# Optimization experiments

Hardware: AMD Instinct MI355X
Metric: run time of the kernel (lower is better)

The kernel has to match this reference:

```python
import jax, jax.numpy as jnp
import numpy as np

B, N, L, D, H = 2, 2048, 2048, 1024, 16
HD = D // H  # 64


def setup_inputs() -> dict:
    key = jax.random.key(0)
    ks = jax.random.split(key, 12)
    s = 0.02
    return {
        "x_q": jax.random.normal(ks[0], (B, N, D), jnp.float32),
        "x_kv": jax.random.normal(ks[1], (B, L, D), jnp.float32),
        "pad_mask": jax.random.randint(ks[2], (B, L), 0, 2) > 0,
        "wq": jax.random.normal(ks[3], (D, D), jnp.float32) * s,
        "bq": jnp.zeros((D,), jnp.float32),
        "wk": jax.random.normal(ks[4], (D, D), jnp.float32) * s,
        "bk": jnp.zeros((D,), jnp.float32),
        "wv": jax.random.normal(ks[5], (D, D), jnp.float32) * s,
        "bv": jnp.zeros((D,), jnp.float32),
        "wo": jax.random.normal(ks[6], (D, D), jnp.float32) * s,
        "bo": jnp.zeros((D,), jnp.float32),
    }


def reference(x_q, x_kv, pad_mask, wq, bq, wk, bk, wv, bv, wo, bo):
    scale = HD ** -0.5
    # projections: (B, S, D) -> (B, H, S, HD)
    def split_heads(x):
        return x.reshape(x.shape[0], x.shape[1], H, HD).transpose(0, 2, 1, 3)
    q = split_heads(x_q @ wq + bq) * scale
    k = split_heads(x_kv @ wk + bk)
    v = split_heads(x_kv @ wv + bv)
    attn = jnp.einsum('bhic,bhjc->bhij', q, k)  # (B, H, N, L)
    neg = -jnp.finfo(attn.dtype).max
    attn = jnp.where(pad_mask[:, None, None, :], neg, attn)
    attn = jax.nn.softmax(attn, axis=-1)
    o = jnp.einsum('bhij,bhjc->bhic', attn, v)  # (B, H, N, HD)
    o = o.transpose(0, 2, 1, 3).reshape(B, N, D)
    return o @ wo + bo
```

## Files before the change

kernel.cpp:

```cpp
#include <hip/hip_runtime.h>
#include <hip/hip_bf16.h>
#include <math.h>

typedef __bf16 bf16;
typedef __attribute__((ext_vector_type(8))) __bf16 bf16x8;
typedef __attribute__((ext_vector_type(4))) __bf16 bf16x4;
typedef __attribute__((ext_vector_type(4))) float floatx4;
typedef __attribute__((ext_vector_type(16))) float floatx16;

#define BB 2
#define NN 2048
#define LL 2048
#define DD 1024
#define HH 16
#define HDD 64

#define QSCALE (0.125f * 1.44269504f)
#define PCLAMP 21.66f
#define MBIAS  (-100000.0f)

__device__ __forceinline__ void async16(const bf16* g, bf16* l) {
  __builtin_amdgcn_global_load_lds((const __attribute__((address_space(1))) void*)(g),
                                   (__attribute__((address_space(3))) void*)(l), 16, 0, 0);
}

__device__ __forceinline__ unsigned cvtpk(float a, float b) {
  unsigned r;
  asm("v_cvt_pk_bf16_f32 %0, %1, %2" : "=v"(r) : "v"(a), "v"(b));
  return r;
}

__device__ __forceinline__ void plswap(unsigned &x, unsigned &y) {
  auto r = __builtin_amdgcn_permlane32_swap(x, y, false, false);
  x = (unsigned)r[0];
  y = (unsigned)r[1];
}

__device__ __forceinline__ bf16x8 mk_frag(unsigned w0, unsigned w1, unsigned w2, unsigned w3) {
  union { unsigned u[4]; bf16x8 b; } f;
  f.u[0] = w0; f.u[1] = w1; f.u[2] = w2; f.u[3] = w3;
  return f.b;
}

__global__ __launch_bounds__(256) void prep_kernel(
    const float* __restrict__ xq, const float* __restrict__ xkv,
    bf16* __restrict__ Xqb, bf16* __restrict__ Xkvb, int nconv, int elemsEach,
    const float* __restrict__ W0, const float* __restrict__ W1,
    const float* __restrict__ W2, const float* __restrict__ W3,
    bf16* __restrict__ T0, bf16* __restrict__ T1,
    bf16* __restrict__ T2, bf16* __restrict__ T3,
    const unsigned* __restrict__ mask, float* __restrict__ biasF)
{
  __shared__ bf16 Tb[64][72];
  const int bid = blockIdx.x;
  const int t = threadIdx.x;

  if (bid < nconv) {
    const int half = nconv >> 1;
    const float* s = (bid < half) ? xq : xkv;
    bf16* d = (bid < half) ? Xqb : Xkvb;
    int gid = (bid < half) ? bid : bid - half;
    int idx = (gid * 256 + t) * 8;
    if (idx >= elemsEach) return;
    floatx4 a = *(const floatx4*)&s[idx];
    floatx4 b = *(const floatx4*)&s[idx + 4];
    bf16x8 o;
#pragma unroll
    for (int e = 0; e < 4; e++) { o[e] = (bf16)a[e]; o[4 + e] = (bf16)b[e]; }
    *(bf16x8*)&d[idx] = o;
    return;
  }
  if (bid < nconv + 1024) {
    const int wb = bid - nconv;
    const int which = wb >> 8;
    const float* W = which == 0 ? W0 : which == 1 ? W1 : which == 2 ? W2 : W3;
    bf16*       T = which == 0 ? T0 : which == 1 ? T1 : which == 2 ? T2 : T3;
    const int tile = wb & 255;
    const int k0 = (tile >> 4) * 64, n0 = (tile & 15) * 64;
    const int r = t >> 2;
    const int c = (t & 3) * 16;
    const float* Wr = W + (size_t)(k0 + r) * 1024 + n0 + c;
    floatx4 f0 = *(const floatx4*)(Wr + 0);
    floatx4 f1 = *(const floatx4*)(Wr + 4);
    floatx4 f2 = *(const floatx4*)(Wr + 8);
    floatx4 f3 = *(const floatx4*)(Wr + 12);
#pragma unroll
    for (int e = 0; e < 4; e++) {
      Tb[c + e][r]      = (bf16)f0[e];
      Tb[c + 4 + e][r]  = (bf16)f1[e];
      Tb[c + 8 + e][r]  = (bf16)f2[e];
      Tb[c + 12 + e][r] = (bf16)f3[e];
    }
    __syncthreads();
    bf16* Tr = T + (size_t)(n0 + r) * 1024 + k0 + c;
    *(bf16x8*)&Tr[0] = *(const bf16x8*)&Tb[r][c];
    *(bf16x8*)&Tr[8] = *(const bf16x8*)&Tb[r][c + 8];
    return;
  }
  __shared__ int hasBig, hasFloat;
  if (t == 0) { hasBig = 0; hasFloat = 0; }
  __syncthreads();
  int big = 0, flt = 0;
  for (int idx = t; idx < 1024; idx += 256) {
    unsigned v = mask[idx];
    if (v == 0x3F800000u) flt = 1;
    else if (v > 1u) big = 1;
  }
  if (big) atomicOr(&hasBig, 1);
  if (flt) atomicOr(&hasFloat, 1);
  __syncthreads();
  const int mode = hasFloat ? 2 : (hasBig ? 1 : 0);
  for (int k = t * 16; k < t * 16 + 16; k++) {
    bool m;
    if (mode == 0)      m = ((const int*)mask)[k] != 0;
    else if (mode == 1) m = ((const unsigned char*)mask)[k] != 0;
    else                m = ((const float*)mask)[k] != 0.0f;
    biasF[k] = m ? MBIAS : 0.0f;
  }
}

template <typename TC>
__device__ __forceinline__ void gemm_body32(
    int bx, const bf16* __restrict__ A, const bf16* __restrict__ Wt,
    const float* __restrict__ bias, TC* __restrict__ C, float scale, int transv)
{
  __shared__ bf16 As[128 * 64];
  __shared__ bf16 Bs[128 * 64];

  const int tm = bx >> 3, tn = bx & 7;
  const int m0 = tm * 128, n0 = tn * 128;
  const int t = threadIdx.x;
  const int w = t >> 6, l = t & 63;
  const int col = l & 31, half = l >> 5;
  const int wm = (w >> 1) * 64, wn = (w & 1) * 64;
  const int sr  = t >> 3;
  const int scl = (t & 7) * 8;
  const int scs = (((t & 7) ^ (sr & 7)) * 8);
  const int csw = col & 7;

  floatx16 acc[2][2];
#pragma unroll
  for (int mi = 0; mi < 2; mi++)
#pragma unroll
    for (int ni = 0; ni < 2; ni++)
#pragma unroll
      for (int e = 0; e < 16; e++) acc[mi][ni][e] = 0.0f;

  for (int k0 = 0; k0 < 1024; k0 += 64) {
    __syncthreads();
#pragma unroll
    for (int j = 0; j < 4; j++)
      async16(&A[(size_t)(m0 + j * 32 + sr) * 1024 + k0 + scs], &As[(j * 32 + sr) * 64 + scl]);
#pragma unroll
    for (int j = 0; j < 4; j++)
      async16(&Wt[(size_t)(n0 + j * 32 + sr) * 1024 + k0 + scs], &Bs[(j * 32 + sr) * 64 + scl]);
    __syncthreads();
#pragma unroll
    for (int kk = 0; kk < 4; kk++) {
      const int ch = ((kk * 2 + half) ^ csw) * 8;
      bf16x8 af[2], bfr[2];
#pragma unroll
      for (int mi = 0; mi < 2; mi++)
        af[mi] = *(const bf16x8*)&As[(wm + mi * 32 + col) * 64 + ch];
#pragma unroll
      for (int ni = 0; ni < 2; ni++)
        bfr[ni] = *(const bf16x8*)&Bs[(wn + ni * 32 + col) * 64 + ch];
#pragma unroll
      for (int mi = 0; mi < 2; mi++)
#pragma unroll
        for (int ni = 0; ni < 2; ni++)
          acc[mi][ni] = __builtin_amdgcn_mfma_f32_32x32x16_bf16(af[mi], bfr[ni], acc[mi][ni], 0, 0, 0);
    }
  }
#pragma unroll
  for (int ni = 0; ni < 2; ni++) {
    int colg = n0 + wn + ni * 32 + col;
    float bv = bias[colg];
#pragma unroll
    for (int mi = 0; mi < 2; mi++) {
      int rbase = m0 + wm + mi * 32 + half * 4;
      if (transv) {
#pragma unroll
        for (int g = 0; g < 4; g++) {
          int key0 = rbase + g * 8;
          int bb = key0 >> 11, key = key0 & 2047;
          bf16x4 v4;
#pragma unroll
          for (int r = 0; r < 4; r++) v4[r] = (bf16)(acc[mi][ni][g * 4 + r] + bv);
          *(bf16x4*)&((bf16*)C)[(size_t)bb * (DD * (size_t)LL) + (size_t)colg * LL + key] = v4;
        }
      } else {
#pragma unroll
        for (int g = 0; g < 4; g++)
#pragma unroll
          for (int r = 0; r < 4; r++)
            C[(size_t)(rbase + g * 8 + r) * 1024 + colg] = (TC)((acc[mi][ni][g * 4 + r] + bv) * scale);
      }
    }
  }
}

__global__ __launch_bounds__(256) void qkv_gemm32(
    const bf16* __restrict__ Xq, const bf16* __restrict__ Xkv,
    const bf16* __restrict__ Wtq, const bf16* __restrict__ Wtk, const bf16* __restrict__ Wtv,
    const float* __restrict__ bq, const float* __restrict__ bk, const float* __restrict__ bv,
    bf16* __restrict__ Qp, bf16* __restrict__ Kp, bf16* __restrict__ VtG, int shift)
{
  const int bid = blockIdx.x;
  const int which = bid >> shift;
  const int bx = bid & ((1 << shift) - 1);
  if (which == 0)      gemm_body32<bf16>(bx, Xq,  Wtq, bq, Qp,  QSCALE, 0);
  else if (which == 1) gemm_body32<bf16>(bx, Xkv, Wtk, bk, Kp,  1.0f,   0);
  else                 gemm_body32<bf16>(bx, Xkv, Wtv, bv, VtG, 1.0f,   1);
}

__global__ __launch_bounds__(256) void out_gemm(
    const bf16* __restrict__ A, const bf16* __restrict__ Wt,
    const float* __restrict__ bias, float* __restrict__ C)
{
  __shared__ bf16 As[128 * 64];
  __shared__ bf16 Bs[64 * 64];

  const int bx = blockIdx.x;
  const int tm = bx >> 4, tn = bx & 15;
  const int m0 = tm * 128, n0 = tn * 64;
  const int t = threadIdx.x;
  const int w = t >> 6, l = t & 63;
  const int q = l >> 4, i = l & 15;
  const int wm = (w >> 1) * 64, wn = (w & 1) * 32;
  const int sr  = t >> 3;
  const int scl = (t & 7) * 8;
  const int scs = (((t & 7) ^ (sr & 7)) * 8);
  const int isw = i & 7;

  const floatx4 zero = {0.f, 0.f, 0.f, 0.f};
  floatx4 acc[4][2];
#pragma unroll
  for (int mi = 0; mi < 4; mi++)
#pragma unroll
    for (int ni = 0; ni < 2; ni++) acc[mi][ni] = zero;

  for (int k0 = 0; k0 < 1024; k0 += 64) {
    __syncthreads();
#pragma unroll
    for (int j = 0; j < 4; j++)
      async16(&A[(size_t)(m0 + j * 32 + sr) * 1024 + k0 + scs], &As[(j * 32 + sr) * 64 + scl]);
#pragma unroll
    for (int j = 0; j < 2; j++)
      async16(&Wt[(size_t)(n0 + j * 32 + sr) * 1024 + k0 + scs], &Bs[(j * 32 + sr) * 64 + scl]);
    __syncthreads();
#pragma unroll
    for (int ks = 0; ks < 2; ks++) {
      const int ch = ((ks * 4 + q) ^ isw) * 8;
      bf16x8 af[4], bfr[2];
#pragma unroll
      for (int mi = 0; mi < 4; mi++)
        af[mi] = *(const bf16x8*)&As[(wm + mi * 16 + i) * 64 + ch];
#pragma unroll
      for (int ni = 0; ni < 2; ni++)
        bfr[ni] = *(const bf16x8*)&Bs[(wn + ni * 16 + i) * 64 + ch];
#pragma unroll
      for (int mi = 0; mi < 4; mi++)
#pragma unroll
        for (int ni = 0; ni < 2; ni++)
          acc[mi][ni] = __builtin_amdgcn_mfma_f32_16x16x32_bf16(af[mi], bfr[ni], acc[mi][ni], 0, 0, 0);
    }
  }
#pragma unroll
  for (int ni = 0; ni < 2; ni++) {
    int colg = n0 + wn + ni * 16 + i;
    float bv = bias[colg];
#pragma unroll
    for (int mi = 0; mi < 4; mi++) {
      int row = m0 + wm + mi * 16 + q * 4;
#pragma unroll
      for (int r = 0; r < 4; r++)
        C[(size_t)(row + r) * 1024 + colg] = acc[mi][ni][r] + bv;
    }
  }
}

__device__ __forceinline__ void attn_tile(
    const bf16* __restrict__ Kg, const bf16* __restrict__ Vg,
    const float* __restrict__ biasFb, int ktn,
    const bf16* Kc, const bf16* Vc, bf16* Kn, bf16* Vn,
    int sr, int scl, int scs, int col, int hi, int lsw,
    const bf16x8* qfrag, floatx4 (*pb)[4], floatx16* oacc, float& psum)
{
  async16(&Kg[(size_t)(ktn + sr) * DD + scs],      Kn + sr * 64 + scl);
  async16(&Kg[(size_t)(ktn + sr + 32) * DD + scs], Kn + (sr + 32) * 64 + scl);
  async16(&Vg[(size_t)sr * LL + ktn + scs],        Vn + sr * 64 + scl);
  async16(&Vg[(size_t)(sr + 32) * LL + ktn + scs], Vn + (sr + 32) * 64 + scl);

  floatx16 sacc[2];
#pragma unroll
  for (int kb = 0; kb < 2; kb++)
#pragma unroll
    for (int g = 0; g < 4; g++)
#pragma unroll
      for (int rr = 0; rr < 4; rr++)
        sacc[kb][g * 4 + rr] = pb[kb][g][rr];

#pragma unroll
  for (int kb = 0; kb < 2; kb++)
#pragma unroll
    for (int dc = 0; dc < 4; dc++) {
      bf16x8 kf = *(const bf16x8*)&Kc[(kb * 32 + col) * 64 + ((dc * 2 + hi) ^ lsw) * 8];
      sacc[kb] = __builtin_amdgcn_mfma_f32_32x32x16_bf16(kf, qfrag[dc], sacc[kb], 0, 0, 0);
    }

#pragma unroll
  for (int kb = 0; kb < 2; kb++)
#pragma unroll
    for (int g = 0; g < 4; g++)
      pb[kb][g] = *(const floatx4*)&biasFb[ktn + kb * 32 + g * 8 + hi * 4];

  bf16x8 pfrag[4];
#pragma unroll
  for (int kb = 0; kb < 2; kb++)
#pragma unroll
    for (int hh = 0; hh < 2; hh++) {
      float pv[8];
#pragma unroll
      for (int e = 0; e < 8; e++) {
        float p = __builtin_amdgcn_exp2f(fminf(sacc[kb][hh * 8 + e], PCLAMP));
        psum += p;
        pv[e] = p;
      }
      unsigned a0 = cvtpk(pv[0], pv[1]);
      unsigned a1 = cvtpk(pv[2], pv[3]);
      unsigned b0 = cvtpk(pv[4], pv[5]);
      unsigned b1 = cvtpk(pv[6], pv[7]);
      plswap(a0, b0);
      plswap(a1, b1);
      pfrag[kb * 2 + hh] = mk_frag(a0, a1, b0, b1);
    }

#pragma unroll
  for (int db = 0; db < 2; db++)
#pragma unroll
    for (int kc = 0; kc < 4; kc++) {
      bf16x8 vf = *(const bf16x8*)&Vc[(db * 32 + col) * 64 + ((kc * 2 + hi) ^ lsw) * 8];
      oacc[db] = __builtin_amdgcn_mfma_f32_32x32x16_bf16(vf, pfrag[kc], oacc[db], 0, 0, 0);
    }
}

__global__ __launch_bounds__(256) void attn_kernel(
    const bf16* __restrict__ Q, const bf16* __restrict__ K,
    const bf16* __restrict__ Vt, const float* __restrict__ biasF,
    bf16* __restrict__ O, int hbits)
{
  __shared__ bf16 Kbuf[2][64 * 64];
  __shared__ bf16 Vbuf[2][64 * 64];

  const int bid = blockIdx.x;
  const int qt = bid >> hbits;
  const int hb = bid & ((1 << hbits) - 1);
  const int h  = (hbits == 5) ? (hb >> 1) : hb;
  const int b  = (hbits == 5) ? (hb & 1) : 0;
  const int t = threadIdx.x;
  const int w = t >> 6, lane = t & 63;
  const int col = lane & 31;
  const int hi  = lane >> 5;
  const int lsw = lane & 7;

  const bf16* Qb = Q  + (size_t)b * (NN * DD) + h * HDD;
  const bf16* Kb = K  + (size_t)b * (LL * DD) + h * HDD;
  const bf16* Vb = Vt + (size_t)b * (DD * (size_t)LL) + (size_t)(h * HDD) * LL;
  const float* biasFb = biasF + b * LL;

  const int qrow = qt * 128 + w * 32;

  bf16x8 qfrag[4];
#pragma unroll
  for (int dc = 0; dc < 4; dc++)
    qfrag[dc] = *(const bf16x8*)&Qb[(size_t)(qrow + col) * DD + dc * 16 + hi * 8];

  floatx16 oacc[2];
#pragma unroll
  for (int db = 0; db < 2; db++)
#pragma unroll
    for (int e = 0; e < 16; e++) oacc[db][e] = 0.0f;
  float psum = 0.0f;

  const int sr  = t >> 3;
  const int scl = (t & 7) * 8;
  const int scs = ((t & 7) ^ (sr & 7)) * 8;

  async16(&Kb[(size_t)sr * DD + scs],        &Kbuf[0][sr * 64 + scl]);
  async16(&Kb[(size_t)(sr + 32) * DD + scs], &Kbuf[0][(sr + 32) * 64 + scl]);
  async16(&Vb[(size_t)sr * LL + scs],        &Vbuf[0][sr * 64 + scl]);
  async16(&Vb[(size_t)(sr + 32) * LL + scs], &Vbuf[0][(sr + 32) * 64 + scl]);

  floatx4 pb[2][4];
#pragma unroll
  for (int kb = 0; kb < 2; kb++)
#pragma unroll
    for (int g = 0; g < 4; g++)
      pb[kb][g] = *(const floatx4*)&biasFb[kb * 32 + g * 8 + hi * 4];

  __syncthreads();

  const bf16 *Kc = &Kbuf[0][0], *Vc = &Vbuf[0][0];
  bf16 *Kn = &Kbuf[1][0], *Vn = &Vbuf[1][0];

  for (int kt = 0; kt < LL; kt += 64) {
    const int ktn = (kt + 64) & (LL - 1);
    attn_tile(Kb, Vb, biasFb, ktn, Kc, Vc, Kn, Vn,
              sr, scl, scs, col, hi, lsw, qfrag, pb, oacc, psum);
    const bf16* tk = Kc; Kc = Kn; Kn = (bf16*)tk;
    const bf16* tv = Vc; Vc = Vn; Vn = (bf16*)tv;
    __syncthreads();
  }

  psum += __shfl_xor(psum, 32, 64);
  float inv = 1.0f / fmaxf(psum, 1e-30f);

  bf16* Ob = O + (size_t)b * (NN * DD) + h * HDD;
#pragma unroll
  for (int db = 0; db < 2; db++)
#pragma unroll
    for (int g = 0; g < 4; g++) {
      bf16x4 v4;
#pragma unroll
      for (int rr = 0; rr < 4; rr++) v4[rr] = (bf16)(oacc[db][g * 4 + rr] * inv);
      *(bf16x4*)&Ob[(size_t)(qrow + col) * DD + db * 32 + g * 8 + hi * 4] = v4;
    }
}

extern "C" void kernel_launch(void* const* d_in, const int* in_sizes, int n_in,
                              void* d_out, int out_size, void* d_ws, size_t ws_size,
                              hipStream_t stream)
{
  const float* x_q  = (const float*)d_in[0];
  const float* x_kv = (const float*)d_in[1];
  const void*  pad  = d_in[2];
  const float* wq = (const float*)d_in[3];
  const float* bq = (const float*)d_in[4];
  const float* wk = (const float*)d_in[5];
  const float* bk = (const float*)d_in[6];
  const float* wv = (const float*)d_in[7];
  const float* bv = (const float*)d_in[8];
  const float* wo = (const float*)d_in[9];
  const float* bo = (const float*)d_in[10];
  float* out = (float*)d_out;

  char* ws = (char*)d_ws;
  const size_t MB = (size_t)1 << 20;
  const size_t fullElems = (size_t)BB * NN * DD;
  const size_t batchElems = (size_t)NN * DD;

  if (ws_size >= 49 * MB) {
    bf16* Xqb   = (bf16*)(ws);
    bf16* Xkvb  = (bf16*)(ws + 8 * MB);
    bf16* Wtq   = (bf16*)(ws + 16 * MB);
    bf16* Wtk   = (bf16*)(ws + 18 * MB);
    bf16* Wtv   = (bf16*)(ws + 20 * MB);
    bf16* Wto   = (bf16*)(ws + 22 * MB);
    bf16* Qp    = (bf16*)(ws + 24 * MB);
    bf16* Kp    = (bf16*)(ws + 32 * MB);
    bf16* VtG   = (bf16*)(ws + 40 * MB);
    float* biasF = (float*)(ws + 48 * MB);
    bf16* Op    = Xqb;

    prep_kernel<<<5121, 256, 0, stream>>>(x_q, x_kv, Xqb, Xkvb, 4096, (int)fullElems,
                                          wq, wk, wv, wo, Wtq, Wtk, Wtv, Wto,
                                          (const unsigned*)pad, biasF);
    qkv_gemm32<<<768, 256, 0, stream>>>(Xqb, Xkvb, Wtq, Wtk, Wtv, bq, bk, bv, Qp, Kp, VtG, 8);
    attn_kernel<<<512, 256, 0, stream>>>(Qp, Kp, VtG, biasF, Op, 5);
    out_gemm<<<512, 256, 0, stream>>>(Op, Wto, bo, out);
  } else {
    bf16* Wtq   = (bf16*)(ws);
    bf16* Wtk   = (bf16*)(ws + 2 * MB);
    bf16* Wtv   = (bf16*)(ws + 4 * MB);
    bf16* Wto   = (bf16*)(ws + 6 * MB);
    bf16* Xqb   = (bf16*)(ws + 8 * MB);
    bf16* Xkvb  = (bf16*)(ws + 12 * MB);
    bf16* Qp    = (bf16*)(ws + 16 * MB);
    bf16* Kp    = (bf16*)(ws + 20 * MB);
    bf16* VtG   = (bf16*)(ws + 24 * MB);
    float* biasF = (float*)(ws + 28 * MB);
    bf16* Op    = Xqb;

    for (int b = 0; b < BB; b++) {
      if (b == 0)
        prep_kernel<<<3073, 256, 0, stream>>>(x_q, x_kv, Xqb, Xkvb, 2048, (int)batchElems,
                                              wq, wk, wv, wo, Wtq, Wtk, Wtv, Wto,
                                              (const unsigned*)pad, biasF);
      else
        prep_kernel<<<2048, 256, 0, stream>>>(x_q + b * batchElems, x_kv + b * batchElems,
                                              Xqb, Xkvb, 2048, (int)batchElems,
                                              wq, wk, wv, wo, Wtq, Wtk, Wtv, Wto,
                                              (const unsigned*)pad, biasF);
      qkv_gemm32<<<384, 256, 0, stream>>>(Xqb, Xkvb, Wtq, Wtk, Wtv, bq, bk, bv, Qp, Kp, VtG, 7);
      attn_kernel<<<256, 256, 0, stream>>>(Qp, Kp, VtG, biasF + b * LL, Op, 4);
      out_gemm<<<256, 256, 0, stream>>>(Op, Wto, bo, out + b * batchElems);
    }
  }
}
```

Before: 234.8 us.

## Software-pipeline attention loop with 4-slot K/V ring and deferred PV

Replaces the double-buffered attention loop with a four-slot LDS ring that prefetches two tiles ahead. The loop is restructured so that iteration k runs QK for tile k and then PV for tile k-1, with the softmax of tile k producing fragments consumed next iteration. The MFMA phases are also wrapped in s_setprio raises. The aim is to overlap softmax exp work and global loads with matrix-core work, at the cost of twice the LDS footprint and more live registers, which may reduce occupancy.

```diff
diff --git a/kernel.cpp b/kernel.cpp
--- a/kernel.cpp
+++ b/kernel.cpp
@@ -280,78 +280,13 @@
   }
 }
 
-__device__ __forceinline__ void attn_tile(
-    const bf16* __restrict__ Kg, const bf16* __restrict__ Vg,
-    const float* __restrict__ biasFb, int ktn,
-    const bf16* Kc, const bf16* Vc, bf16* Kn, bf16* Vn,
-    int sr, int scl, int scs, int col, int hi, int lsw,
-    const bf16x8* qfrag, floatx4 (*pb)[4], floatx16* oacc, float& psum)
-{
-  async16(&Kg[(size_t)(ktn + sr) * DD + scs],      Kn + sr * 64 + scl);
-  async16(&Kg[(size_t)(ktn + sr + 32) * DD + scs], Kn + (sr + 32) * 64 + scl);
-  async16(&Vg[(size_t)sr * LL + ktn + scs],        Vn + sr * 64 + scl);
-  async16(&Vg[(size_t)(sr + 32) * LL + ktn + scs], Vn + (sr + 32) * 64 + scl);
-
-  floatx16 sacc[2];
-#pragma unroll
-  for (int kb = 0; kb < 2; kb++)
-#pragma unroll
-    for (int g = 0; g < 4; g++)
-#pragma unroll
-      for (int rr = 0; rr < 4; rr++)
-        sacc[kb][g * 4 + rr] = pb[kb][g][rr];
-
-#pragma unroll
-  for (int kb = 0; kb < 2; kb++)
-#pragma unroll
-    for (int dc = 0; dc < 4; dc++) {
-      bf16x8 kf = *(const bf16x8*)&Kc[(kb * 32 + col) * 64 + ((dc * 2 + hi) ^ lsw) * 8];
-      sacc[kb] = __builtin_amdgcn_mfma_f32_32x32x16_bf16(kf, qfrag[dc], sacc[kb], 0, 0, 0);
-    }
-
-#pragma unroll
-  for (int kb = 0; kb < 2; kb++)
-#pragma unroll
-    for (int g = 0; g < 4; g++)
-      pb[kb][g] = *(const floatx4*)&biasFb[ktn + kb * 32 + g * 8 + hi * 4];
-
-  bf16x8 pfrag[4];
-#pragma unroll
-  for (int kb = 0; kb < 2; kb++)
-#pragma unroll
-    for (int hh = 0; hh < 2; hh++) {
-      float pv[8];
-#pragma unroll
-      for (int e = 0; e < 8; e++) {
-        float p = __builtin_amdgcn_exp2f(fminf(sacc[kb][hh * 8 + e], PCLAMP));
-        psum += p;
-        pv[e] = p;
-      }
-      unsigned a0 = cvtpk(pv[0], pv[1]);
-      unsigned a1 = cvtpk(pv[2], pv[3]);
-      unsigned b0 = cvtpk(pv[4], pv[5]);
-      unsigned b1 = cvtpk(pv[6], pv[7]);
-      plswap(a0, b0);
-      plswap(a1, b1);
-      pfrag[kb * 2 + hh] = mk_frag(a0, a1, b0, b1);
-    }
-
-#pragma unroll
-  for (int db = 0; db < 2; db++)
-#pragma unroll
-    for (int kc = 0; kc < 4; kc++) {
-      bf16x8 vf = *(const bf16x8*)&Vc[(db * 32 + col) * 64 + ((kc * 2 + hi) ^ lsw) * 8];
-      oacc[db] = __builtin_amdgcn_mfma_f32_32x32x16_bf16(vf, pfrag[kc], oacc[db], 0, 0, 0);
-    }
-}
-
 __global__ __launch_bounds__(256) void attn_kernel(
     const bf16* __restrict__ Q, const bf16* __restrict__ K,
     const bf16* __restrict__ Vt, const float* __restrict__ biasF,
     bf16* __restrict__ O, int hbits)
 {
-  __shared__ bf16 Kbuf[2][64 * 64];
-  __shared__ bf16 Vbuf[2][64 * 64];
+  __shared__ bf16 Kbuf[4][64 * 64];
+  __shared__ bf16 Vbuf[4][64 * 64];
 
   const int bid = blockIdx.x;
   const int qt = bid >> hbits;
@@ -387,31 +322,100 @@
   const int scl = (t & 7) * 8;
   const int scs = ((t & 7) ^ (sr & 7)) * 8;
 
-  async16(&Kb[(size_t)sr * DD + scs],        &Kbuf[0][sr * 64 + scl]);
-  async16(&Kb[(size_t)(sr + 32) * DD + scs], &Kbuf[0][(sr + 32) * 64 + scl]);
-  async16(&Vb[(size_t)sr * LL + scs],        &Vbuf[0][sr * 64 + scl]);
-  async16(&Vb[(size_t)(sr + 32) * LL + scs], &Vbuf[0][(sr + 32) * 64 + scl]);
+  auto STAGE = [&](int tile, int slot) {
+    const int k0 = tile * 64;
+    async16(&Kb[(size_t)(k0 + sr) * DD + scs],        &Kbuf[slot][sr * 64 + scl]);
+    async16(&Kb[(size_t)(k0 + sr + 32) * DD + scs],   &Kbuf[slot][(sr + 32) * 64 + scl]);
+    async16(&Vb[(size_t)sr * LL + k0 + scs],          &Vbuf[slot][sr * 64 + scl]);
+    async16(&Vb[(size_t)(sr + 32) * LL + k0 + scs],   &Vbuf[slot][(sr + 32) * 64 + scl]);
+  };
 
   floatx4 pb[2][4];
+  bf16x8 pfp[4];
+  floatx16 sacc[2];
+
+  auto QK = [&](int slot) {
+#pragma unroll
+    for (int kb = 0; kb < 2; kb++)
+#pragma unroll
+      for (int g = 0; g < 4; g++)
+#pragma unroll
+        for (int rr = 0; rr < 4; rr++)
+          sacc[kb][g * 4 + rr] = pb[kb][g][rr];
+    __builtin_amdgcn_s_setprio(1);
+#pragma unroll
+    for (int kb = 0; kb < 2; kb++)
+#pragma unroll
+      for (int dc = 0; dc < 4; dc++) {
+        bf16x8 kf = *(const bf16x8*)&Kbuf[slot][(kb * 32 + col) * 64 + ((dc * 2 + hi) ^ lsw) * 8];
+        sacc[kb] = __builtin_amdgcn_mfma_f32_32x32x16_bf16(kf, qfrag[dc], sacc[kb], 0, 0, 0);
+      }
+  };
+
+  auto PV = [&](int slot) {
+#pragma unroll
+    for (int db = 0; db < 2; db++)
+#pragma unroll
+      for (int kc = 0; kc < 4; kc++) {
+        bf16x8 vf = *(const bf16x8*)&Vbuf[slot][(db * 32 + col) * 64 + ((kc * 2 + hi) ^ lsw) * 8];
+        oacc[db] = __builtin_amdgcn_mfma_f32_32x32x16_bf16(vf, pfp[kc], oacc[db], 0, 0, 0);
+      }
+    __builtin_amdgcn_s_setprio(0);
+  };
+
+  auto SOFTMAX = [&](int nextTile) {
+#pragma unroll
+    for (int kb = 0; kb < 2; kb++)
+#pragma unroll
+      for (int hh = 0; hh < 2; hh++) {
+        float pv[8];
+#pragma unroll
+        for (int e = 0; e < 8; e++) {
+          float p = __builtin_amdgcn_exp2f(fminf(sacc[kb][hh * 8 + e], PCLAMP));
+          psum += p;
+          pv[e] = p;
+        }
+        unsigned a0 = cvtpk(pv[0], pv[1]);
+        unsigned a1 = cvtpk(pv[2], pv[3]);
+        unsigned b0 = cvtpk(pv[4], pv[5]);
+        unsigned b1 = cvtpk(pv[6], pv[7]);
+        plswap(a0, b0);
+        plswap(a1, b1);
+        pfp[kb * 2 + hh] = mk_frag(a0, a1, b0, b1);
+      }
+    const int kn = (nextTile & 31) * 64;
+#pragma unroll
+    for (int kb = 0; kb < 2; kb++)
+#pragma unroll
+      for (int g = 0; g < 4; g++)
+        pb[kb][g] = *(const floatx4*)&biasFb[kn + kb * 32 + g * 8 + hi * 4];
+  };
+
+  STAGE(0, 0);
+  STAGE(1, 1);
 #pragma unroll
   for (int kb = 0; kb < 2; kb++)
 #pragma unroll
     for (int g = 0; g < 4; g++)
       pb[kb][g] = *(const floatx4*)&biasFb[kb * 32 + g * 8 + hi * 4];
-
   __syncthreads();
 
-  const bf16 *Kc = &Kbuf[0][0], *Vc = &Vbuf[0][0];
-  bf16 *Kn = &Kbuf[1][0], *Vn = &Vbuf[1][0];
-
-  for (int kt = 0; kt < LL; kt += 64) {
-    const int ktn = (kt + 64) & (LL - 1);
-    attn_tile(Kb, Vb, biasFb, ktn, Kc, Vc, Kn, Vn,
-              sr, scl, scs, col, hi, lsw, qfrag, pb, oacc, psum);
-    const bf16* tk = Kc; Kc = Kn; Kn = (bf16*)tk;
-    const bf16* tv = Vc; Vc = Vn; Vn = (bf16*)tv;
+  STAGE(2, 2);
+  QK(0);
+  __builtin_amdgcn_s_setprio(0);
+  SOFTMAX(1);
+  __syncthreads();
+
+  const int NT = LL / 64;
+  for (int kt = 1; kt < NT; kt++) {
+    if (kt + 2 < NT) STAGE(kt + 2, (kt + 2) & 3);
+    QK(kt & 3);
+    PV((kt - 1) & 3);
+    SOFTMAX(kt + 1);
     __syncthreads();
   }
+  __builtin_amdgcn_s_setprio(1);
+  PV((NT - 1) & 3);
 
   psum += __shfl_xor(psum, 32, 64);
   float inv = 1.0f / fmaxf(psum, 1e-30f);
```

After: 235.7 us. No clear change (+0.4%).
